# Kernel tuning notes

Measured on AMD Instinct MI355X. Metric: run time of the kernel, lower is better.

The kernel has to match this reference:

```python
import jax, jax.numpy as jnp
import numpy as np
from jax import lax

HEADS = 8

# Haar-lifting 4x4 matrices from nlwt_init / inlwt_init
U1P1 = jnp.array([[-0.5, -0.5, -0.5, 0.5], [0.5, -0.5, 0.5, 0.5], [0.5, 0.5, -0.5, 0.5], [0.5, -0.5, -0.5, -0.5]], jnp.float32)
U2P2 = jnp.array([[-1., 1., 1., -1.], [-1., -1., -1., -1.], [-1., -1., 1., 1.], [1., -1., 1., -1.]], jnp.float32)
P2U2 = jnp.array([[-1., -1., -1., 1.], [1., -1., -1., -1.], [1., -1., 1., 1.], [-1., -1., 1., -1.]], jnp.float32)
P1U1 = jnp.array([[-0.125, 0.125, 0.125, 0.125], [-0.125, -0.125, 0.125, -0.125], [-0.125, 0.125, -0.125, -0.125], [0.125, 0.125, 0.125, -0.125]], jnp.float32)


def conv1x1(x, w):
    # w: [out_ch, in_ch]
    return jnp.einsum('oi,bihw->bohw', w, x)


def dwconv3(x, w):
    # depthwise 3x3, w: [C,1,3,3]
    return lax.conv_general_dilated(x, w, (1, 1), [(1, 1), (1, 1)],
                                    dimension_numbers=('NCHW', 'OIHW', 'NCHW'),
                                    feature_group_count=x.shape[1])


def layernorm_c(x, w, b):
    # WithBias LayerNorm over channel dim (to_3d normalizes last dim == c)
    mu = jnp.mean(x, axis=1, keepdims=True)
    var = jnp.var(x, axis=1, keepdims=True)
    return (x - mu) / jnp.sqrt(var + 1e-5) * w[None, :, None, None] + b[None, :, None, None]


def attention(x, temperature, qkv_w, qkv_dw_w, proj_w):
    b, c, h, w = x.shape
    qkv = dwconv3(conv1x1(x, qkv_w), qkv_dw_w)
    q, k, v = jnp.split(qkv, 3, axis=1)
    hd = lambda t: t.reshape(b, HEADS, c // HEADS, h * w)
    q, k, v = hd(q), hd(k), hd(v)
    q = q / jnp.maximum(jnp.linalg.norm(q, axis=-1, keepdims=True), 1e-12)
    k = k / jnp.maximum(jnp.linalg.norm(k, axis=-1, keepdims=True), 1e-12)
    attn = jax.nn.softmax(jnp.einsum('bhcn,bhdn->bhcd', q, k) * temperature, axis=-1)
    out = jnp.einsum('bhcd,bhdn->bhcn', attn, v).reshape(b, c, h, w)
    return conv1x1(out, proj_w)


def ffn(x, pin_w, dw_w, pout_w):
    y = dwconv3(conv1x1(x, pin_w), dw_w)
    y1, y2 = jnp.split(y, 2, axis=1)
    return conv1x1(jax.nn.gelu(y1, approximate=False) * y2, pout_w)


def tblock(x, ln1_w, ln1_b, temperature, qkv_w, qkv_dw_w, proj_w, ln2_w, ln2_b, pin_w, ffn_dw_w, pout_w):
    x = x + attention(layernorm_c(x, ln1_w, ln1_b), temperature, qkv_w, qkv_dw_w, proj_w)
    x = x + ffn(layernorm_c(x, ln2_w, ln2_b), pin_w, ffn_dw_w, pout_w)
    return x


def nlwt(x):
    # lifting wavelet decompose (nlwt_init), vectorized im2col via reshape
    b, c, h, w = x.shape
    h1, w1 = h // 2, w // 2
    col = x.reshape(b, c, h1, 2, w1, 2).transpose(0, 1, 3, 5, 2, 4).reshape(b, c, 4, h1 * w1)
    x1 = jnp.einsum('ij,bcjn->bcin', U1P1, col).reshape(b, c, 4, h1, w1)
    t1 = x1[:, :, 0]
    t2 = jnp.roll(x1[:, :, 1], -1, axis=2)
    t3 = jnp.roll(x1[:, :, 2], -1, axis=3)
    t4 = jnp.roll(x1[:, :, 3], (-1, -1), axis=(2, 3))
    x1 = jnp.stack([t1, t2, t3, t4], axis=2).reshape(b, c, 4, h1 * w1)
    x2 = jnp.einsum('ij,bcjn->bcin', U2P2, x1).reshape(b, c, 4, h1, w1)
    return x2[:, :, 0], x2[:, :, 1], x2[:, :, 2], x2[:, :, 3]


def inlwt(A, B, C, D):
    # lifting wavelet reconstruct (inlwt_init), vectorized col2im via reshape
    b, c, h1, w1 = A.shape
    Y1 = jnp.stack([A, B, C, D], axis=2).reshape(b, c, 4, h1 * w1)
    Y2 = jnp.einsum('ij,bcjn->bcin', P2U2, Y1).reshape(b, c, 4, h1, w1)
    t1 = Y2[:, :, 0]
    t2 = jnp.roll(Y2[:, :, 1], 1, axis=2)
    t3 = jnp.roll(Y2[:, :, 2], 1, axis=3)
    t4 = jnp.roll(Y2[:, :, 3], (1, 1), axis=(2, 3))
    Y2 = jnp.stack([t1, t2, t3, t4], axis=2).reshape(b, c, 4, h1 * w1)
    Y3 = jnp.einsum('ij,bcjn->bcin', P1U1, Y2).reshape(b, c, 2, 2, h1, w1)
    return Y3.transpose(0, 1, 4, 2, 5, 3).reshape(b, c, 2 * h1, 2 * w1)


def gfm(x1, x2, ca_w1, ca_w2, sa_w, sa_b):
    Cc = x1.shape[1]
    cat = jnp.concatenate([x1, x2], axis=1)  # [b, 2C, h, w]
    avg = jnp.mean(cat, axis=(2, 3), keepdims=True)
    mx = jnp.max(cat, axis=(2, 3), keepdims=True)
    mlp = lambda t: conv1x1(jax.nn.relu(conv1x1(t, ca_w1)), ca_w2)
    cw = jax.nn.sigmoid(mlp(avg) + mlp(mx))  # [b, 2C, 1, 1]
    cw = cw.reshape(-1, 2, Cc)[:, :, :, None, None]
    out = cw[:, 0] * x1 + cw[:, 1] * x2
    savg = jnp.mean(out, axis=1, keepdims=True)
    smax = jnp.max(out, axis=1, keepdims=True)
    sa = lax.conv_general_dilated(jnp.concatenate([savg, smax], axis=1), sa_w, (1, 1), [(3, 3), (3, 3)],
                                  dimension_numbers=('NCHW', 'OIHW', 'NCHW')) + sa_b[None, :, None, None]
    return jax.nn.sigmoid(sa) * out


def setup_inputs() -> dict:
    key = jax.random.key(0)
    ks = jax.random.split(key, 16)
    B, C, H, W = 2, 48, 256, 256
    hidden = int(C * 2.66)  # 127
    s = 0.05
    return {
        'x': jax.random.normal(ks[0], (B, C, H, W), jnp.float32),
        'ln1_w': jnp.ones((C,), jnp.float32),
        'ln1_b': jnp.zeros((C,), jnp.float32),
        'temperature': jnp.ones((HEADS, 1, 1), jnp.float32),
        'qkv_w': jax.random.normal(ks[1], (3 * C, C), jnp.float32) * s,
        'qkv_dw_w': jax.random.normal(ks[2], (3 * C, 1, 3, 3), jnp.float32) * s,
        'proj_w': jax.random.normal(ks[3], (C, C), jnp.float32) * s,
        'ln2_w': jnp.ones((C,), jnp.float32),
        'ln2_b': jnp.zeros((C,), jnp.float32),
        'pin_w': jax.random.normal(ks[4], (2 * hidden, C), jnp.float32) * s,
        'ffn_dw_w': jax.random.normal(ks[5], (2 * hidden, 1, 3, 3), jnp.float32) * s,
        'pout_w': jax.random.normal(ks[6], (C, hidden), jnp.float32) * s,
        'ca_w1': jax.random.normal(ks[7], (2 * C // 16, 2 * C), jnp.float32) * s,
        'ca_w2': jax.random.normal(ks[8], (2 * C, 2 * C // 16), jnp.float32) * s,
        'sa_w': jax.random.normal(ks[9], (1, 2, 7, 7), jnp.float32) * s,
        'sa_b': jnp.zeros((1,), jnp.float32),
    }


def reference(x, ln1_w, ln1_b, temperature, qkv_w, qkv_dw_w, proj_w, ln2_w, ln2_b, pin_w, ffn_dw_w, pout_w, ca_w1, ca_w2, sa_w, sa_b):
    tb = lambda t: tblock(t, ln1_w, ln1_b, temperature, qkv_w, qkv_dw_w, proj_w, ln2_w, ln2_b, pin_w, ffn_dw_w, pout_w)
    branch1 = tb(x)
    A, Bh, Ch, Dh = nlwt(x)
    branch2 = inlwt(tb(A), Bh, Ch, Dh)
    return gfm(branch1, branch2, ca_w1, ca_w2, sa_w, sa_b)
```

## Files before the change

### kernel.cpp

```cpp
#include <hip/hip_runtime.h>
#include <math.h>

namespace {

constexpr int BB   = 2;
constexpr int CC   = 48;
constexpr int NHEAD= 8;
constexpr int CPH  = 6;
constexpr int HID  = 127;
constexpr int QKVC = 144;
constexpr int PINC = 254;
constexpr int N1   = 256*256;
constexpr int N2   = 128*128;
constexpr size_t PS2 = (size_t)BB*CC*N2;
constexpr size_t NB1 = (size_t)BB*CC*N1;

using short8  = __attribute__((ext_vector_type(8))) short;
using floatx4 = __attribute__((ext_vector_type(4))) float;

__device__ __forceinline__ float b2f(unsigned short u) {
    unsigned int x = ((unsigned int)u) << 16;
    float f; __builtin_memcpy(&f, &x, 4); return f;
}
__device__ __forceinline__ unsigned short f2b(float f) {
    unsigned int x; __builtin_memcpy(&x, &f, 4);
    unsigned int r = (x + 0x7FFFu + ((x >> 16) & 1u)) >> 16;
    return (unsigned short)r;
}
__device__ __forceinline__ unsigned int pack2(float lo, float hi) {
    return (unsigned int)f2b(lo) | ((unsigned int)f2b(hi) << 16);
}

__device__ __forceinline__ float gelu_t(float x) {
    float z = 1.5957691216057308f * (x + 0.044715f * x * x * x);
    float e = __expf(z);
    return x * (1.0f - 1.0f / (e + 1.0f));
}

__global__ void k_zero(float* __restrict__ p, int n)
{
    int i = blockIdx.x*256 + threadIdx.x;
    if (i < n) p[i] = 0.f;
}

__global__ void k_repw(const float* __restrict__ w, float* __restrict__ wt, int O, int K)
{
    int i = blockIdx.x*256 + threadIdx.x;
    if (i < O*K) {
        int c = i / O, oc = i - c*O;
        wt[c*O + oc] = w[oc*K + c];
    }
}

template<int OCR, int OCT>
__global__ void k_packw_mfma(const float* __restrict__ w, unsigned short* __restrict__ wf)
{
    int i = blockIdx.x*256 + threadIdx.x;
    if (i >= OCT*2*64) return;
    int lane = i & 63, ts = i >> 6;
    int s = ts & 1, t = ts >> 1;
    int oc = t*16 + (lane & 15);
    int kb = s*32 + (lane >> 4)*8;
    float v[8];
#pragma unroll
    for (int j = 0; j < 8; ++j) {
        int k = kb + j;
        v[j] = (oc < OCR && k < 48) ? w[oc*48 + k] : 0.f;
    }
    uint4 o;
    o.x = pack2(v[0], v[1]); o.y = pack2(v[2], v[3]);
    o.z = pack2(v[4], v[5]); o.w = pack2(v[6], v[7]);
    *(uint4*)(wf + (size_t)i*8) = o;
}

__global__ __launch_bounds__(256) void k_ln_t(const float* __restrict__ X,
                       const float* __restrict__ lw, const float* __restrict__ lb,
                       unsigned short* __restrict__ xh, int Ns)
{
    int g = blockIdx.x*256 + threadIdx.x;
    int half = Ns >> 1;
    int b = g >= half ? 1 : 0;
    int pp = (g - b*half)*2;
    const float* xb = X + (size_t)b*CC*Ns + pp;
    float v0[CC], v1[CC];
    float s0=0.f, s20=0.f, s1=0.f, s21=0.f;
#pragma unroll
    for (int c = 0; c < CC; ++c) {
        float2 v = *(const float2*)(xb + (size_t)c*Ns);
        v0[c]=v.x; v1[c]=v.y;
        s0 += v.x; s20 = fmaf(v.x,v.x,s20);
        s1 += v.y; s21 = fmaf(v.y,v.y,s21);
    }
    float mu0 = s0*(1.0f/CC), mu1 = s1*(1.0f/CC);
    float i0 = 1.0f/sqrtf(s20*(1.0f/CC)-mu0*mu0+1e-5f);
    float i1 = 1.0f/sqrtf(s21*(1.0f/CC)-mu1*mu1+1e-5f);
    unsigned short* r0 = xh + ((size_t)b*Ns + pp)*48;
    unsigned short* r1 = r0 + 48;
#pragma unroll
    for (int j = 0; j < 6; ++j) {
        uint4 o0, o1;
        float y[8], z[8];
#pragma unroll
        for (int e = 0; e < 8; ++e) {
            int c = j*8 + e;
            float w = lw[c], bb2 = lb[c];
            y[e] = (v0[c]-mu0)*i0*w + bb2;
            z[e] = (v1[c]-mu1)*i1*w + bb2;
        }
        o0.x = pack2(y[0],y[1]); o0.y = pack2(y[2],y[3]);
        o0.z = pack2(y[4],y[5]); o0.w = pack2(y[6],y[7]);
        o1.x = pack2(z[0],z[1]); o1.y = pack2(z[2],z[3]);
        o1.z = pack2(z[4],z[5]); o1.w = pack2(z[6],z[7]);
        *(uint4*)(r0 + j*8) = o0;
        *(uint4*)(r1 + j*8) = o1;
    }
}

template<int OCR, int OCT>
__global__ __launch_bounds__(256) void k_conv_mfma(const unsigned short* __restrict__ xh,
                       const unsigned short* __restrict__ wf,
                       unsigned short* __restrict__ out, int Ns)
{
    int wid = (blockIdx.x*256 + (int)threadIdx.x) >> 6;
    int lane = threadIdx.x & 63;
    int tpb = Ns >> 4;
    int b = wid / tpb, pxt = wid - b*tpb;
    int px0 = pxt << 4;
    int col = lane & 15, grp = lane >> 4;
    const unsigned short* xb = xh + ((size_t)b*Ns + px0 + col)*48 + grp*8;
    short8 b0 = *(const short8*)(xb);
    short8 b1 = *(const short8*)(xb + 32);
    unsigned short* ob = out + (size_t)b*OCR*Ns + px0 + col;
    int ocb0 = grp*4;
#pragma unroll
    for (int t = 0; t < OCT; ++t) {
        floatx4 acc = {};
        short8 a0 = *(const short8*)(wf + (size_t)((t*2+0)*64 + lane)*8);
        short8 a1 = *(const short8*)(wf + (size_t)((t*2+1)*64 + lane)*8);
        acc = __builtin_amdgcn_mfma_f32_16x16x32_bf16(a0, b0, acc, 0, 0, 0);
        acc = __builtin_amdgcn_mfma_f32_16x16x32_bf16(a1, b1, acc, 0, 0, 0);
#pragma unroll
        for (int r = 0; r < 4; ++r) {
            int oc = t*16 + ocb0 + r;
            if (OCR % 16 == 0 || oc < OCR)
                ob[(size_t)oc*Ns] = f2b(acc[r]);
        }
    }
}

__device__ __forceinline__ void load_row10(const unsigned short* __restrict__ p,
                                           bool lok, bool rrok, float (&f)[10])
{
    uint4 cv = *(const uint4*)p;
    unsigned int u0=cv.x,u1=cv.y,u2=cv.z,u3=cv.w;
    f[1]=b2f((unsigned short)(u0&0xffffu)); f[2]=b2f((unsigned short)(u0>>16));
    f[3]=b2f((unsigned short)(u1&0xffffu)); f[4]=b2f((unsigned short)(u1>>16));
    f[5]=b2f((unsigned short)(u2&0xffffu)); f[6]=b2f((unsigned short)(u2>>16));
    f[7]=b2f((unsigned short)(u3&0xffffu)); f[8]=b2f((unsigned short)(u3>>16));
    f[0] = lok  ? b2f(p[-1]) : 0.f;
    f[9] = rrok ? b2f(p[8])  : 0.f;
}

__device__ __forceinline__ void dw2x8(const unsigned short* __restrict__ plane,
                                      const float* __restrict__ w9,
                                      int y0, int x0, int Hs, int Ws, float (&acc)[2][8])
{
#pragma unroll
    for (int r = 0; r < 2; ++r)
#pragma unroll
        for (int i = 0; i < 8; ++i) acc[r][i] = 0.f;
    bool lok = x0 > 0, rrok = x0 + 8 < Ws;
#pragma unroll
    for (int ir = 0; ir < 4; ++ir) {
        int r = y0 + ir - 1;
        if (r < 0 || r >= Hs) continue;
        float f[10];
        load_row10(plane + (size_t)r*Ws + x0, lok, rrok, f);
#pragma unroll
        for (int ky = 0; ky < 3; ++ky) {
            int orow = ir - ky;
            if (orow < 0 || orow > 1) continue;
            float w0 = w9[ky*3], w1 = w9[ky*3+1], w2 = w9[ky*3+2];
#pragma unroll
            for (int i = 0; i < 8; ++i)
                acc[orow][i] = fmaf(f[i], w0, fmaf(f[i+1], w1, fmaf(f[i+2], w2, acc[orow][i])));
        }
    }
}

__global__ __launch_bounds__(256) void k_dw3v(const unsigned short* __restrict__ in,
                      const float* __restrict__ w,
                      unsigned short* __restrict__ out, int Hs, int Ws, int lgNgt, int lgWq)
{
    int g = blockIdx.x*256 + threadIdx.x;
    int t = g & ((1<<lgNgt)-1), bc = g >> lgNgt;
    int c = bc % QKVC;
    int y0 = (t >> lgWq) << 1, x0 = (t & ((1<<lgWq)-1)) << 3;
    int Ns = Hs*Ws;
    float acc[2][8];
    dw2x8(in + (size_t)bc*Ns, w + c*9, y0, x0, Hs, Ws, acc);
    unsigned short* ob = out + (size_t)bc*Ns + (size_t)y0*Ws + x0;
#pragma unroll
    for (int r = 0; r < 2; ++r) {
        uint4 o;
        o.x = pack2(acc[r][0],acc[r][1]); o.y = pack2(acc[r][2],acc[r][3]);
        o.z = pack2(acc[r][4],acc[r][5]); o.w = pack2(acc[r][6],acc[r][7]);
        *(uint4*)(ob + (size_t)r*Ws) = o;
    }
}

__global__ __launch_bounds__(256) void k_dwgate(const unsigned short* __restrict__ pin,
                         const float* __restrict__ dww,
                         unsigned short* __restrict__ gate, int Hs, int Ws, int lgNgt, int lgWq)
{
    int g = blockIdx.x*256 + threadIdx.x;
    int t = g & ((1<<lgNgt)-1), bc = g >> lgNgt;
    int b = bc / HID, c = bc - b*HID;
    int y0 = (t >> lgWq) << 1, x0 = (t & ((1<<lgWq)-1)) << 3;
    int Ns = Hs*Ws;
    float a1[2][8], a2[2][8];
    dw2x8(pin + ((size_t)b*PINC + c)*Ns,       dww + c*9,       y0, x0, Hs, Ws, a1);
    dw2x8(pin + ((size_t)b*PINC + HID + c)*Ns, dww + (c+HID)*9, y0, x0, Hs, Ws, a2);
    unsigned short* ob = gate + (size_t)bc*Ns + (size_t)y0*Ws + x0;
#pragma unroll
    for (int r = 0; r < 2; ++r) {
        uint4 o;
        o.x = pack2(gelu_t(a1[r][0])*a2[r][0], gelu_t(a1[r][1])*a2[r][1]);
        o.y = pack2(gelu_t(a1[r][2])*a2[r][2], gelu_t(a1[r][3])*a2[r][3]);
        o.z = pack2(gelu_t(a1[r][4])*a2[r][4], gelu_t(a1[r][5])*a2[r][5]);
        o.w = pack2(gelu_t(a1[r][6])*a2[r][6], gelu_t(a1[r][7])*a2[r][7]);
        *(uint4*)(ob + (size_t)r*Ws) = o;
    }
}

__global__ __launch_bounds__(256) void k_qk_stats(const unsigned short* __restrict__ qkvd,
                                                  float* __restrict__ st, int Ns)
{
    const int NBLK = 32;
    int bh = blockIdx.x / NBLK, blk = blockIdx.x % NBLK;
    int b = bh / NHEAD, h = bh % NHEAD;
    const unsigned short* qb = qkvd + ((size_t)b*QKVC + h*CPH)*Ns;
    const unsigned short* kb = qkvd + ((size_t)b*QKVC + 48 + h*CPH)*Ns;
    float vals[48];
#pragma unroll
    for (int i = 0; i < 48; ++i) vals[i] = 0.f;
    for (int n = blk*512 + (int)threadIdx.x*2; n < Ns; n += NBLK*512) {
        float q0[CPH], q1[CPH], k0[CPH], k1[CPH];
#pragma unroll
        for (int i = 0; i < CPH; ++i) {
            unsigned int qu = *(const unsigned int*)(qb + (size_t)i*Ns + n);
            unsigned int ku = *(const unsigned int*)(kb + (size_t)i*Ns + n);
            q0[i] = b2f((unsigned short)(qu & 0xffffu)); q1[i] = b2f((unsigned short)(qu >> 16));
            k0[i] = b2f((unsigned short)(ku & 0xffffu)); k1[i] = b2f((unsigned short)(ku >> 16));
        }
#pragma unroll
        for (int i = 0; i < CPH; ++i) {
            vals[i]   = fmaf(q0[i],q0[i], fmaf(q1[i],q1[i], vals[i]));
            vals[6+i] = fmaf(k0[i],k0[i], fmaf(k1[i],k1[i], vals[6+i]));
        }
#pragma unroll
        for (int i = 0; i < CPH; ++i)
#pragma unroll
            for (int j = 0; j < CPH; ++j)
                vals[12+i*6+j] = fmaf(q0[i],k0[j], fmaf(q1[i],k1[j], vals[12+i*6+j]));
    }
    __shared__ float red[4][48];
    int lane = threadIdx.x & 63, wave = threadIdx.x >> 6;
#pragma unroll
    for (int i = 0; i < 48; ++i) {
        float v = vals[i];
#pragma unroll
        for (int off = 32; off > 0; off >>= 1) v += __shfl_down(v, off);
        if (lane == 0) red[wave][i] = v;
    }
    __syncthreads();
    if ((int)threadIdx.x < 48) {
        int i = threadIdx.x;
        float v = red[0][i] + red[1][i] + red[2][i] + red[3][i];
        float* dst;
        if (i < 6)       dst = st + b*48 + h*CPH + i;
        else if (i < 12) dst = st + 96 + b*48 + h*CPH + (i-6);
        else             dst = st + 192 + (b*NHEAD+h)*36 + (i-12);
        atomicAdd(dst, v);
    }
}

__global__ void k_attn(const float* __restrict__ st, const float* __restrict__ temp,
                       const float* __restrict__ projw, float* __restrict__ Mt)
{
    int t = threadIdx.x;
    if (t >= BB*NHEAD) return;
    int b = t / NHEAD, h = t % NHEAD;
    const float* sqq = st + b*48 + h*CPH;
    const float* sqk = st + 96 + b*48 + h*CPH;
    const float* g   = st + 192 + (b*NHEAD+h)*36;
    float T = temp[h];
    float nq[CPH], nk[CPH];
#pragma unroll
    for (int i = 0; i < CPH; ++i) {
        nq[i] = fmaxf(sqrtf(sqq[i]), 1e-12f);
        nk[i] = fmaxf(sqrtf(sqk[i]), 1e-12f);
    }
    float a[CPH][CPH];
#pragma unroll
    for (int c = 0; c < CPH; ++c) {
        float l[CPH]; float m = -1e30f;
#pragma unroll
        for (int d = 0; d < CPH; ++d) {
            l[d] = g[c*6+d] / (nq[c]*nk[d]) * T;
            m = fmaxf(m, l[d]);
        }
        float ssum = 0.f;
#pragma unroll
        for (int d = 0; d < CPH; ++d) { l[d] = expf(l[d]-m); ssum += l[d]; }
        float r = 1.0f/ssum;
#pragma unroll
        for (int d = 0; d < CPH; ++d) a[c][d] = l[d]*r;
    }
    float* mb = Mt + b*CC*CC;
#pragma unroll
    for (int d = 0; d < CPH; ++d) {
        for (int oc = 0; oc < CC; ++oc) {
            float m = 0.f;
#pragma unroll
            for (int c = 0; c < CPH; ++c)
                m = fmaf(projw[oc*CC + h*CPH + c], a[c][d], m);
            mb[(h*CPH+d)*CC + oc] = m;
        }
    }
}

__global__ __launch_bounds__(256) void k_av_proj(const unsigned short* __restrict__ qkvd,
                          const float* __restrict__ Mt, const float* __restrict__ X,
                          float* __restrict__ x1, int Ns)
{
    int g = blockIdx.x*256 + threadIdx.x;
    int half = Ns >> 1;
    int b = g >= half ? 1 : 0;
    int pp = (g - b*half)*2;
    int ocb = blockIdx.y * 16;
    const unsigned short* vb = qkvd + ((size_t)b*QKVC + 96)*Ns + pp;
    const float* mt = Mt + b*CC*CC;
    float a0[16], a1[16];
#pragma unroll
    for (int i = 0; i < 16; ++i) { a0[i] = 0.f; a1[i] = 0.f; }
#pragma unroll
    for (int c0 = 0; c0 < CC; c0 += 8) {
        unsigned int gv[8];
#pragma unroll
        for (int u = 0; u < 8; ++u)
            gv[u] = *(const unsigned int*)(vb + (size_t)(c0+u)*Ns);
#pragma unroll
        for (int u = 0; u < 8; ++u) {
            float t0 = b2f((unsigned short)(gv[u] & 0xffffu));
            float t1 = b2f((unsigned short)(gv[u] >> 16));
            const float* wr = mt + (c0+u)*CC + ocb;
#pragma unroll
            for (int i = 0; i < 16; ++i) {
                float w = wr[i];
                a0[i] = fmaf(t0, w, a0[i]);
                a1[i] = fmaf(t1, w, a1[i]);
            }
        }
    }
    const float* xb = X + (size_t)b*CC*Ns + pp;
    float* ob = x1 + (size_t)b*CC*Ns + pp;
#pragma unroll
    for (int i = 0; i < 16; ++i) {
        float2 xv = *(const float2*)(xb + (size_t)(ocb+i)*Ns);
        float2 o; o.x = xv.x + a0[i]; o.y = xv.y + a1[i];
        *(float2*)(ob + (size_t)(ocb+i)*Ns) = o;
    }
}

template<int U>
__device__ __forceinline__ void pout_chunk(const unsigned short* __restrict__ gb, int c0, int Ns,
                                           const float* __restrict__ wt, int ocb,
                                           float (&a0)[16], float (&a1)[16])
{
    unsigned int gv[U];
#pragma unroll
    for (int u = 0; u < U; ++u)
        gv[u] = *(const unsigned int*)(gb + (size_t)(c0+u)*Ns);
#pragma unroll
    for (int u = 0; u < U; ++u) {
        float t0 = b2f((unsigned short)(gv[u] & 0xffffu));
        float t1 = b2f((unsigned short)(gv[u] >> 16));
        const float* wr = wt + (c0+u)*48 + ocb;
#pragma unroll
        for (int i = 0; i < 16; ++i) {
            float w = wr[i];
            a0[i] = fmaf(t0, w, a0[i]);
            a1[i] = fmaf(t1, w, a1[i]);
        }
    }
}

__global__ __launch_bounds__(256) void k_pout(const unsigned short* __restrict__ gate,
                       const float* __restrict__ wt, const float* __restrict__ x1,
                       float* __restrict__ out, int Ns)
{
    int g = blockIdx.x*256 + threadIdx.x;
    int half = Ns >> 1;
    int b = g >= half ? 1 : 0;
    int pp = (g - b*half)*2;
    int ocb = blockIdx.y * 16;
    const unsigned short* gb = gate + (size_t)b*HID*Ns + pp;
    float a0[16], a1[16];
#pragma unroll
    for (int i = 0; i < 16; ++i) { a0[i] = 0.f; a1[i] = 0.f; }
    int c = 0;
    for (; c + 8 <= HID; c += 8)
        pout_chunk<8>(gb, c, Ns, wt, ocb, a0, a1);
    pout_chunk<7>(gb, c, Ns, wt, ocb, a0, a1);
    const float* xb = x1 + (size_t)b*CC*Ns + pp;
    float* ob = out + (size_t)b*CC*Ns + pp;
#pragma unroll
    for (int i = 0; i < 16; ++i) {
        float2 xv = *(const float2*)(xb + (size_t)(ocb+i)*Ns);
        float2 o; o.x = xv.x + a0[i]; o.y = xv.y + a1[i];
        *(float2*)(ob + (size_t)(ocb+i)*Ns) = o;
    }
}

__global__ __launch_bounds__(256) void k_nlwt(const float* __restrict__ X, float* __restrict__ A4)
{
    int g = blockIdx.x*256 + threadIdx.x;
    int n = g & (N2-1); int bc = g >> 14;
    int h1 = n >> 7, w1 = n & 127;
    int hb = (h1+1)&127, wb = (w1+1)&127;
    const float* xp = X + (size_t)bc * N1;
    float t1, t2, t3, t4;
    {
        int y=h1, z=w1;
        float c0=xp[(2*y)*256+2*z], c1=xp[(2*y)*256+2*z+1], c2=xp[(2*y+1)*256+2*z], c3=xp[(2*y+1)*256+2*z+1];
        t1 = 0.5f*(-c0 - c1 - c2 + c3);
    }
    {
        int y=hb, z=w1;
        float c0=xp[(2*y)*256+2*z], c1=xp[(2*y)*256+2*z+1], c2=xp[(2*y+1)*256+2*z], c3=xp[(2*y+1)*256+2*z+1];
        t2 = 0.5f*( c0 - c1 + c2 + c3);
    }
    {
        int y=h1, z=wb;
        float c0=xp[(2*y)*256+2*z], c1=xp[(2*y)*256+2*z+1], c2=xp[(2*y+1)*256+2*z], c3=xp[(2*y+1)*256+2*z+1];
        t3 = 0.5f*( c0 + c1 - c2 + c3);
    }
    {
        int y=hb, z=wb;
        float c0=xp[(2*y)*256+2*z], c1=xp[(2*y)*256+2*z+1], c2=xp[(2*y+1)*256+2*z], c3=xp[(2*y+1)*256+2*z+1];
        t4 = 0.5f*( c0 - c1 - c2 - c3);
    }
    size_t o = (size_t)bc*N2 + n;
    A4[o]           = -t1 + t2 + t3 - t4;
    A4[PS2 + o]     = -t1 - t2 - t3 - t4;
    A4[2*PS2 + o]   = -t1 - t2 + t3 + t4;
    A4[3*PS2 + o]   =  t1 - t2 + t3 - t4;
}

__global__ __launch_bounds__(256) void k_inlwt(const float* __restrict__ Ain, const float* __restrict__ A4,
                        float* __restrict__ out)
{
    int g = blockIdx.x*256 + threadIdx.x;
    int n = g & (N2-1); int bc = g >> 14;
    int h1 = n >> 7, w1 = n & 127;
    int hm = (h1-1)&127, wm = (w1-1)&127;
    const float* I0 = Ain + (size_t)bc*N2;
    const float* I1 = A4 + PS2   + (size_t)bc*N2;
    const float* I2 = A4 + 2*PS2 + (size_t)bc*N2;
    const float* I3 = A4 + 3*PS2 + (size_t)bc*N2;
    int i00 = h1*128+w1, i10 = hm*128+w1, i01 = h1*128+wm, i11 = hm*128+wm;
    float t1, t2, t3, t4;
    { float a=I0[i00], b2=I1[i00], c2=I2[i00], d2=I3[i00]; t1 = -a - b2 - c2 + d2; }
    { float a=I0[i10], b2=I1[i10], c2=I2[i10], d2=I3[i10]; t2 =  a - b2 - c2 - d2; }
    { float a=I0[i01], b2=I1[i01], c2=I2[i01], d2=I3[i01]; t3 =  a - b2 + c2 + d2; }
    { float a=I0[i11], b2=I1[i11], c2=I2[i11], d2=I3[i11]; t4 = -a - b2 + c2 - d2; }
    float y00 = 0.125f*(-t1 + t2 + t3 + t4);
    float y01 = 0.125f*(-t1 - t2 + t3 - t4);
    float y10 = 0.125f*(-t1 + t2 - t3 - t4);
    float y11 = 0.125f*( t1 + t2 + t3 - t4);
    float* ob = out + (size_t)bc * N1;
    int oy = h1*2, ox = w1*2;
    ob[(size_t)oy*256 + ox]       = y00;
    ob[(size_t)oy*256 + ox + 1]   = y01;
    ob[(size_t)(oy+1)*256 + ox]   = y10;
    ob[(size_t)(oy+1)*256 + ox+1] = y11;
}

constexpr int CSEG = 8;
__global__ __launch_bounds__(256) void k_chstat_part(const float* __restrict__ b1, const float* __restrict__ b2,
                         float* __restrict__ ps, float* __restrict__ pm)
{
    int bc = blockIdx.x;
    int seg = blockIdx.y;
    int b = bc / 96, ch = bc % 96;
    const float* src = (ch < 48 ? b1 + ((size_t)b*CC + ch)*N1
                                : b2 + ((size_t)b*CC + (ch-48))*N1) + (size_t)seg*(N1/CSEG);
    const float4* s4 = (const float4*)src;
    float s = 0.f, m = -1e30f;
    for (int i = threadIdx.x; i < N1/CSEG/4; i += 256) {
        float4 v = s4[i];
        s += v.x+v.y+v.z+v.w;
        m = fmaxf(m, fmaxf(fmaxf(v.x,v.y), fmaxf(v.z,v.w)));
    }
    int lane = threadIdx.x & 63, wave = threadIdx.x >> 6;
    __shared__ float rs[4], rm[4];
#pragma unroll
    for (int off = 32; off > 0; off >>= 1) {
        s += __shfl_down(s, off);
        m = fmaxf(m, __shfl_down(m, off));
    }
    if (lane == 0) { rs[wave] = s; rm[wave] = m; }
    __syncthreads();
    if (threadIdx.x == 0) {
        ps[bc*CSEG + seg] = rs[0]+rs[1]+rs[2]+rs[3];
        pm[bc*CSEG + seg] = fmaxf(fmaxf(rm[0],rm[1]), fmaxf(rm[2],rm[3]));
    }
}

__global__ void k_chstat_fin(const float* __restrict__ ps, const float* __restrict__ pm,
                             float* __restrict__ avg, float* __restrict__ mxo)
{
    int t = threadIdx.x;
    if (t >= BB*96) return;
    float s = 0.f, m = -1e30f;
#pragma unroll
    for (int j = 0; j < CSEG; ++j) {
        s += ps[t*CSEG+j];
        m = fmaxf(m, pm[t*CSEG+j]);
    }
    avg[t] = s*(1.0f/N1);
    mxo[t] = m;
}

__global__ void k_cw(const float* __restrict__ avg, const float* __restrict__ mx,
                     const float* __restrict__ w1, const float* __restrict__ w2,
                     float* __restrict__ cw)
{
    int t = threadIdx.x;
    if (t >= BB*96) return;
    int b = t / 96, o = t % 96;
    float ta[6], tm[6];
#pragma unroll
    for (int j = 0; j < 6; ++j) {
        float sa = 0.f, sm = 0.f;
        for (int i = 0; i < 96; ++i) {
            float w = w1[j*96+i];
            sa = fmaf(w, avg[b*96+i], sa);
            sm = fmaf(w, mx[b*96+i], sm);
        }
        ta[j] = sa > 0.f ? sa : 0.f;
        tm[j] = sm > 0.f ? sm : 0.f;
    }
    float ua = 0.f, um = 0.f;
#pragma unroll
    for (int j = 0; j < 6; ++j) {
        ua = fmaf(w2[o*6+j], ta[j], ua);
        um = fmaf(w2[o*6+j], tm[j], um);
    }
    float z = ua + um;
    cw[t] = 1.0f/(1.0f+expf(-z));
}

__global__ __launch_bounds__(256) void k_gfm_out(const float* __restrict__ b1, const float* __restrict__ b2,
                          const float* __restrict__ cw, float* __restrict__ ob,
                          float* __restrict__ savg, float* __restrict__ smax)
{
    int g = blockIdx.x*256 + threadIdx.x;
    int b = g >> 16, p = g & (N1-1);
    float s = 0.f, m = -1e30f;
#pragma unroll
    for (int c = 0; c < CC; ++c) {
        size_t idx = ((size_t)b*CC + c)*N1 + p;
        float o = cw[b*96 + c]*b1[idx] + cw[b*96 + 48 + c]*b2[idx];
        ob[idx] = o;
        s += o; m = fmaxf(m, o);
    }
    savg[(size_t)b*N1 + p] = s*(1.0f/CC);
    smax[(size_t)b*N1 + p] = m;
}

__global__ __launch_bounds__(256) void k_final(const float* __restrict__ savg, const float* __restrict__ smax,
                        const float* __restrict__ saw, const float* __restrict__ sab,
                        const float* __restrict__ ob, float* __restrict__ out)
{
    int g = blockIdx.x*256 + threadIdx.x;
    int b = g >> 16, p = g & (N1-1);
    int y = p >> 8, x = p & 255;
    float s = sab[0];
    const float* av = savg + (size_t)b*N1;
    const float* mx = smax + (size_t)b*N1;
#pragma unroll
    for (int ky = 0; ky < 7; ++ky) {
        int yy = y + ky - 3;
        bool yok = (yy >= 0) && (yy < 256);
        int yc = yy < 0 ? 0 : (yy > 255 ? 255 : yy);
#pragma unroll
        for (int kx = 0; kx < 7; ++kx) {
            int xx = x + kx - 3;
            bool ok = yok && (xx >= 0) && (xx < 256);
            int xc = xx < 0 ? 0 : (xx > 255 ? 255 : xx);
            int idx = yc*256 + xc;
            float a = av[idx], m2 = mx[idx];
            s = fmaf(ok ? a  : 0.f, saw[ky*7+kx], s);
            s = fmaf(ok ? m2 : 0.f, saw[49 + ky*7+kx], s);
        }
    }
    float sig = 1.0f/(1.0f+expf(-s));
#pragma unroll
    for (int c = 0; c < CC; ++c) {
        size_t idx = ((size_t)b*CC + c)*N1 + p;
        out[idx] = sig * ob[idx];
    }
}

}

extern "C" void kernel_launch(void* const* d_in, const int* in_sizes, int n_in,
                              void* d_out, int out_size, void* d_ws, size_t ws_size,
                              hipStream_t stream)
{
    const float* x    = (const float*)d_in[0];
    const float* ln1w = (const float*)d_in[1];
    const float* ln1b = (const float*)d_in[2];
    const float* temp = (const float*)d_in[3];
    const float* qkvw = (const float*)d_in[4];
    const float* qkvdw= (const float*)d_in[5];
    const float* projw= (const float*)d_in[6];
    const float* ln2w = (const float*)d_in[7];
    const float* ln2b = (const float*)d_in[8];
    const float* pinw = (const float*)d_in[9];
    const float* ffdw = (const float*)d_in[10];
    const float* poutw= (const float*)d_in[11];
    const float* caw1 = (const float*)d_in[12];
    const float* caw2 = (const float*)d_in[13];
    const float* saw  = (const float*)d_in[14];
    const float* sab  = (const float*)d_in[15];

    float* wsf  = (float*)d_ws;
    float* A4   = wsf;
    float* br1  = A4 + 4*PS2;
    float* br2  = br1 + NB1;
    float* x1b  = br2 + NB1;
    float* tbA  = x1b + NB1;
    float* qkv  = tbA + PS2;
    float* qkvd = qkv + (size_t)BB*QKVC*N1;
    float* stats= qkvd + (size_t)BB*QKVC*N1;
    float* wfqf = stats + 4096;
    float* wfpf = wfqf + 4608;
    float* wor  = wfpf + 8192;
    float* chps = wor + HID*48;
    float* chpm = chps + 192*CSEG;
    float* savg = chpm + 192*CSEG;
    float* smax = savg + (size_t)BB*N1;
    float* Mt   = smax + (size_t)BB*N1;

    unsigned short* wfq = (unsigned short*)wfqf;
    unsigned short* wfp = (unsigned short*)wfpf;

    k_packw_mfma<QKVC, 9><<<(9*2*64+255)/256, 256, 0, stream>>>(qkvw, wfq);
    k_packw_mfma<PINC, 16><<<(16*2*64+255)/256, 256, 0, stream>>>(pinw, wfp);
    k_repw<<<(HID*48+255)/256, 256, 0, stream>>>(poutw, wor, 48, HID);

    auto tb = [&](const float* Xin, float* outp, int Hs, int Ws) {
        int Ns = Hs*Ws;
        int npix = BB*Ns;
        int lgWq = 31 - __builtin_clz(Ws >> 3);
        int lgNgt = (31 - __builtin_clz(Hs >> 1)) + lgWq;
        unsigned short* xhat = (unsigned short*)qkvd;
        k_zero<<<3, 256, 0, stream>>>(stats, 768);
        k_ln_t<<<npix/512, 256, 0, stream>>>(Xin, ln1w, ln1b, xhat, Ns);
        k_conv_mfma<QKVC, 9><<<npix/64, 256, 0, stream>>>(xhat, wfq, (unsigned short*)qkv, Ns);
        k_dw3v<<<(BB*QKVC*(Ns/16))/256, 256, 0, stream>>>((const unsigned short*)qkv, qkvdw,
                                                          (unsigned short*)qkvd, Hs, Ws, lgNgt, lgWq);
        k_qk_stats<<<BB*NHEAD*32, 256, 0, stream>>>((const unsigned short*)qkvd, stats, Ns);
        k_attn<<<1, 64, 0, stream>>>(stats, temp, projw, Mt);
        dim3 g4(npix/512, 3);
        k_av_proj<<<g4, 256, 0, stream>>>((const unsigned short*)qkvd, Mt, Xin, x1b, Ns);
        k_ln_t<<<npix/512, 256, 0, stream>>>(x1b, ln2w, ln2b, xhat, Ns);
        k_conv_mfma<PINC, 16><<<npix/64, 256, 0, stream>>>(xhat, wfp, (unsigned short*)qkv, Ns);
        k_dwgate<<<(BB*HID*(Ns/16)+255)/256, 256, 0, stream>>>((const unsigned short*)qkv, ffdw,
                                                        (unsigned short*)qkvd, Hs, Ws, lgNgt, lgWq);
        dim3 g6(npix/512, 3);
        k_pout<<<g6, 256, 0, stream>>>((const unsigned short*)qkvd, wor, x1b, outp, Ns);
    };

    tb(x, br1, 256, 256);
    k_nlwt<<<(BB*CC*N2)/256, 256, 0, stream>>>(x, A4);
    tb(A4, tbA, 128, 128);
    k_inlwt<<<(BB*CC*N2)/256, 256, 0, stream>>>(tbA, A4, br2);
    dim3 gc(BB*96, CSEG);
    k_chstat_part<<<gc, 256, 0, stream>>>(br1, br2, chps, chpm);
    k_chstat_fin<<<1, 256, 0, stream>>>(chps, chpm, stats + 1344, stats + 1536);
    k_cw<<<1, 256, 0, stream>>>(stats + 1344, stats + 1536, caw1, caw2, stats + 1728);
    k_gfm_out<<<(BB*N1)/256, 256, 0, stream>>>(br1, br2, stats + 1728, x1b, savg, smax);
    k_final<<<(BB*N1)/256, 256, 0, stream>>>(savg, smax, saw, sab, x1b, (float*)d_out);
}
```

Baseline: 427.3 us.

## Merge small kernels, vectorize GFM output and spatial attention to two pixels per thread

```diff
diff --git a/kernel.cpp b/kernel.cpp
--- a/kernel.cpp
+++ b/kernel.cpp
@@ -1,4 +1,5 @@
 #include <hip/hip_runtime.h>
+#include <hip/hip_bf16.h>
 #include <math.h>
 
 namespace {
@@ -23,24 +24,18 @@
     float f; __builtin_memcpy(&f, &x, 4); return f;
 }
 __device__ __forceinline__ unsigned short f2b(float f) {
-    unsigned int x; __builtin_memcpy(&x, &f, 4);
-    unsigned int r = (x + 0x7FFFu + ((x >> 16) & 1u)) >> 16;
-    return (unsigned short)r;
+    __hip_bfloat16 h = __float2bfloat16(f);
+    unsigned short u; __builtin_memcpy(&u, &h, 2); return u;
 }
 __device__ __forceinline__ unsigned int pack2(float lo, float hi) {
-    return (unsigned int)f2b(lo) | ((unsigned int)f2b(hi) << 16);
+    unsigned short a = f2b(lo), b = f2b(hi);
+    return (unsigned int)a | ((unsigned int)b << 16);
 }
 
 __device__ __forceinline__ float gelu_t(float x) {
     float z = 1.5957691216057308f * (x + 0.044715f * x * x * x);
     float e = __expf(z);
     return x * (1.0f - 1.0f / (e + 1.0f));
-}
-
-__global__ void k_zero(float* __restrict__ p, int n)
-{
-    int i = blockIdx.x*256 + threadIdx.x;
-    if (i < n) p[i] = 0.f;
 }
 
 __global__ void k_repw(const float* __restrict__ w, float* __restrict__ wt, int O, int K)
@@ -75,8 +70,12 @@
 
 __global__ __launch_bounds__(256) void k_ln_t(const float* __restrict__ X,
                        const float* __restrict__ lw, const float* __restrict__ lb,
-                       unsigned short* __restrict__ xh, int Ns)
-{
+                       unsigned short* __restrict__ xh, float* __restrict__ stats, int Ns)
+{
+    if (blockIdx.x == 0) {
+        int t = threadIdx.x;
+        stats[t] = 0.f; stats[256+t] = 0.f; stats[512+t] = 0.f;
+    }
     int g = blockIdx.x*256 + threadIdx.x;
     int half = Ns >> 1;
     int b = g >= half ? 1 : 0;
@@ -518,26 +517,23 @@
     }
 }
 
-__global__ void k_chstat_fin(const float* __restrict__ ps, const float* __restrict__ pm,
-                             float* __restrict__ avg, float* __restrict__ mxo)
-{
+__global__ void k_cwfin(const float* __restrict__ ps, const float* __restrict__ pm,
+                        const float* __restrict__ w1, const float* __restrict__ w2,
+                        float* __restrict__ cw)
+{
+    __shared__ float avg[192], mxs[192];
     int t = threadIdx.x;
-    if (t >= BB*96) return;
-    float s = 0.f, m = -1e30f;
-#pragma unroll
-    for (int j = 0; j < CSEG; ++j) {
-        s += ps[t*CSEG+j];
-        m = fmaxf(m, pm[t*CSEG+j]);
-    }
-    avg[t] = s*(1.0f/N1);
-    mxo[t] = m;
-}
-
-__global__ void k_cw(const float* __restrict__ avg, const float* __restrict__ mx,
-                     const float* __restrict__ w1, const float* __restrict__ w2,
-                     float* __restrict__ cw)
-{
-    int t = threadIdx.x;
+    if (t < 192) {
+        float s = 0.f, m = -1e30f;
+#pragma unroll
+        for (int j = 0; j < CSEG; ++j) {
+            s += ps[t*CSEG+j];
+            m = fmaxf(m, pm[t*CSEG+j]);
+        }
+        avg[t] = s*(1.0f/N1);
+        mxs[t] = m;
+    }
+    __syncthreads();
     if (t >= BB*96) return;
     int b = t / 96, o = t % 96;
     float ta[6], tm[6];
@@ -547,7 +543,7 @@
         for (int i = 0; i < 96; ++i) {
             float w = w1[j*96+i];
             sa = fmaf(w, avg[b*96+i], sa);
-            sm = fmaf(w, mx[b*96+i], sm);
+            sm = fmaf(w, mxs[b*96+i], sm);
         }
         ta[j] = sa > 0.f ? sa : 0.f;
         tm[j] = sm > 0.f ? sm : 0.f;
@@ -567,17 +563,25 @@
                           float* __restrict__ savg, float* __restrict__ smax)
 {
     int g = blockIdx.x*256 + threadIdx.x;
-    int b = g >> 16, p = g & (N1-1);
-    float s = 0.f, m = -1e30f;
+    int half = N1 >> 1;
+    int b = g >= half ? 1 : 0;
+    int pp = (g - b*half)*2;
+    float s0 = 0.f, m0 = -1e30f, s1 = 0.f, m1 = -1e30f;
 #pragma unroll
     for (int c = 0; c < CC; ++c) {
-        size_t idx = ((size_t)b*CC + c)*N1 + p;
-        float o = cw[b*96 + c]*b1[idx] + cw[b*96 + 48 + c]*b2[idx];
-        ob[idx] = o;
-        s += o; m = fmaxf(m, o);
-    }
-    savg[(size_t)b*N1 + p] = s*(1.0f/CC);
-    smax[(size_t)b*N1 + p] = m;
+        size_t idx = ((size_t)b*CC + c)*N1 + pp;
+        float2 v1 = *(const float2*)(b1 + idx);
+        float2 v2 = *(const float2*)(b2 + idx);
+        float w1 = cw[b*96 + c], w2 = cw[b*96 + 48 + c];
+        float2 o; o.x = w1*v1.x + w2*v2.x; o.y = w1*v1.y + w2*v2.y;
+        *(float2*)(ob + idx) = o;
+        s0 += o.x; m0 = fmaxf(m0, o.x);
+        s1 += o.y; m1 = fmaxf(m1, o.y);
+    }
+    float2 sv; sv.x = s0*(1.0f/CC); sv.y = s1*(1.0f/CC);
+    float2 mv; mv.x = m0; mv.y = m1;
+    *(float2*)(savg + (size_t)b*N1 + pp) = sv;
+    *(float2*)(smax + (size_t)b*N1 + pp) = mv;
 }
 
 __global__ __launch_bounds__(256) void k_final(const float* __restrict__ savg, const float* __restrict__ smax,
@@ -585,32 +589,43 @@
                         const float* __restrict__ ob, float* __restrict__ out)
 {
     int g = blockIdx.x*256 + threadIdx.x;
-    int b = g >> 16, p = g & (N1-1);
-    int y = p >> 8, x = p & 255;
-    float s = sab[0];
+    int half = N1 >> 1;
+    int b = g >= half ? 1 : 0;
+    int t = g - b*half;
+    int y = t >> 7, x0 = (t & 127) << 1;
     const float* av = savg + (size_t)b*N1;
     const float* mx = smax + (size_t)b*N1;
+    float sb = sab[0];
+    float a0 = sb, a1 = sb;
 #pragma unroll
     for (int ky = 0; ky < 7; ++ky) {
         int yy = y + ky - 3;
-        bool yok = (yy >= 0) && (yy < 256);
-        int yc = yy < 0 ? 0 : (yy > 255 ? 255 : yy);
-#pragma unroll
-        for (int kx = 0; kx < 7; ++kx) {
-            int xx = x + kx - 3;
-            bool ok = yok && (xx >= 0) && (xx < 256);
-            int xc = xx < 0 ? 0 : (xx > 255 ? 255 : xx);
-            int idx = yc*256 + xc;
-            float a = av[idx], m2 = mx[idx];
-            s = fmaf(ok ? a  : 0.f, saw[ky*7+kx], s);
-            s = fmaf(ok ? m2 : 0.f, saw[49 + ky*7+kx], s);
-        }
-    }
-    float sig = 1.0f/(1.0f+expf(-s));
+        if (yy < 0 || yy > 255) continue;
+        const float* ar = av + yy*256;
+        const float* mr = mx + yy*256;
+        float fa[8], fm[8];
+#pragma unroll
+        for (int j = 0; j < 8; ++j) {
+            int xx = x0 - 3 + j;
+            bool ok = (xx >= 0) && (xx < 256);
+            fa[j] = ok ? ar[xx] : 0.f;
+            fm[j] = ok ? mr[xx] : 0.f;
+        }
+#pragma unroll
+        for (int j = 0; j < 7; ++j) {
+            float wa = saw[ky*7+j], wm = saw[49 + ky*7+j];
+            a0 = fmaf(fa[j],   wa, fmaf(fm[j],   wm, a0));
+            a1 = fmaf(fa[j+1], wa, fmaf(fm[j+1], wm, a1));
+        }
+    }
+    float s0 = 1.0f/(1.0f+__expf(-a0));
+    float s1 = 1.0f/(1.0f+__expf(-a1));
+    size_t base = (size_t)b*CC*N1 + (size_t)y*256 + x0;
 #pragma unroll
     for (int c = 0; c < CC; ++c) {
-        size_t idx = ((size_t)b*CC + c)*N1 + p;
-        out[idx] = sig * ob[idx];
+        float2 v = *(const float2*)(ob + base + (size_t)c*N1);
+        float2 o; o.x = v.x*s0; o.y = v.y*s1;
+        *(float2*)(out + base + (size_t)c*N1) = o;
     }
 }
 
@@ -668,8 +683,7 @@
         int lgWq = 31 - __builtin_clz(Ws >> 3);
         int lgNgt = (31 - __builtin_clz(Hs >> 1)) + lgWq;
         unsigned short* xhat = (unsigned short*)qkvd;
-        k_zero<<<3, 256, 0, stream>>>(stats, 768);
-        k_ln_t<<<npix/512, 256, 0, stream>>>(Xin, ln1w, ln1b, xhat, Ns);
+        k_ln_t<<<npix/512, 256, 0, stream>>>(Xin, ln1w, ln1b, xhat, stats, Ns);
         k_conv_mfma<QKVC, 9><<<npix/64, 256, 0, stream>>>(xhat, wfq, (unsigned short*)qkv, Ns);
         k_dw3v<<<(BB*QKVC*(Ns/16))/256, 256, 0, stream>>>((const unsigned short*)qkv, qkvdw,
                                                           (unsigned short*)qkvd, Hs, Ws, lgNgt, lgWq);
@@ -677,7 +691,7 @@
         k_attn<<<1, 64, 0, stream>>>(stats, temp, projw, Mt);
         dim3 g4(npix/512, 3);
         k_av_proj<<<g4, 256, 0, stream>>>((const unsigned short*)qkvd, Mt, Xin, x1b, Ns);
-        k_ln_t<<<npix/512, 256, 0, stream>>>(x1b, ln2w, ln2b, xhat, Ns);
+        k_ln_t<<<npix/512, 256, 0, stream>>>(x1b, ln2w, ln2b, xhat, stats, Ns);
         k_conv_mfma<PINC, 16><<<npix/64, 256, 0, stream>>>(xhat, wfp, (unsigned short*)qkv, Ns);
         k_dwgate<<<(BB*HID*(Ns/16)+255)/256, 256, 0, stream>>>((const unsigned short*)qkv, ffdw,
                                                         (unsigned short*)qkvd, Hs, Ws, lgNgt, lgWq);
@@ -691,8 +705,7 @@
     k_inlwt<<<(BB*CC*N2)/256, 256, 0, stream>>>(tbA, A4, br2);
     dim3 gc(BB*96, CSEG);
     k_chstat_part<<<gc, 256, 0, stream>>>(br1, br2, chps, chpm);
-    k_chstat_fin<<<1, 256, 0, stream>>>(chps, chpm, stats + 1344, stats + 1536);
-    k_cw<<<1, 256, 0, stream>>>(stats + 1344, stats + 1536, caw1, caw2, stats + 1728);
-    k_gfm_out<<<(BB*N1)/256, 256, 0, stream>>>(br1, br2, stats + 1728, x1b, savg, smax);
-    k_final<<<(BB*N1)/256, 256, 0, stream>>>(savg, smax, saw, sab, x1b, (float*)d_out);
-}
+    k_cwfin<<<1, 256, 0, stream>>>(chps, chpm, caw1, caw2, stats + 1728);
+    k_gfm_out<<<(BB*N1/2)/256, 256, 0, stream>>>(br1, br2, stats + 1728, x1b, savg, smax);
+    k_final<<<(BB*N1/2)/256, 256, 0, stream>>>(savg, smax, saw, sab, x1b, (float*)d_out);
+}
```

Measured after the change: 449.8 us. 5.3% more time.
